# Kernel optimization log

Hardware: AMD Instinct MI355X
Metric: run time of the kernel (lower is better)

Reference implementation:

```python
import jax, jax.numpy as jnp
import numpy as np

N_NODES = 500_000
N_EDGES = 8_000_000
N_GRAPHS = 1000


def _mlp(x, w1, b1, w2, b2):
    # Linear -> SELU -> Linear (torch Sequential equivalent)
    return jax.nn.selu(x @ w1 + b1) @ w2 + b2


def setup_inputs() -> dict:
    key = jax.random.key(0)
    ks = jax.random.split(key, 25)
    p = lambda i, shape: jax.random.normal(ks[i], shape, jnp.float32) * 0.1
    return {
        "nodes": jax.random.normal(ks[0], (N_NODES, 1), jnp.float32),
        "edges": jax.random.normal(ks[1], (N_EDGES, 1), jnp.float32),
        "senders": jax.random.randint(ks[2], (N_EDGES,), 0, N_NODES),
        "receivers": jax.random.randint(ks[3], (N_EDGES,), 0, N_NODES),
        "graph_ids": jnp.sort(jax.random.randint(ks[4], (N_NODES,), 0, N_GRAPHS)),
        "num_graphs": N_GRAPHS,
        # permutate_nodes: 2 -> 10 -> 10
        "pn_w1": p(5, (2, 10)), "pn_b1": p(6, (10,)), "pn_w2": p(7, (10, 10)), "pn_b2": p(8, (10,)),
        # update_edges: 11 -> 5 -> 1
        "ue_w1": p(9, (11, 5)), "ue_b1": p(10, (5,)), "ue_w2": p(11, (5, 1)), "ue_b2": p(12, (1,)),
        # permutate_edges: 1 -> 5 -> 10
        "pe_w1": p(13, (1, 5)), "pe_b1": p(14, (5,)), "pe_w2": p(15, (5, 10)), "pe_b2": p(16, (10,)),
        # update_nodes: 11 -> 5 -> 1
        "un_w1": p(17, (11, 5)), "un_b1": p(18, (5,)), "un_w2": p(19, (5, 1)), "un_b2": p(20, (1,)),
        # predict: 11 -> 10 -> 10
        "pr_w1": p(21, (11, 10)), "pr_b1": p(22, (10,)), "pr_w2": p(23, (10, 10)), "pr_b2": p(24, (10,)),
    }


def reference(nodes, edges, pn_w1, pn_b1, pn_w2, pn_b2,
              ue_w1, ue_b1, ue_w2, ue_b2,
              pe_w1, pe_b1, pe_w2, pe_b2,
              un_w1, un_b1, un_w2, un_b2,
              pr_w1, pr_b1, pr_w2, pr_b2,
              senders, receivers, graph_ids, num_graphs):
    # gather node feats to edges: [recv || send] -> (E, 2)
    collected = jnp.concatenate([nodes[receivers], nodes[senders]], axis=-1)
    h1_nodes = _mlp(collected, pn_w1, pn_b1, pn_w2, pn_b2)  # (E, 10)
    h1_edges = edges  # (E, 1)
    for _ in range(3):
        h1_edges = _mlp(jnp.concatenate([h1_edges, h1_nodes], axis=-1),
                        ue_w1, ue_b1, ue_w2, ue_b2)  # (E, 1)
    # edges -> nodes aggregation (sum over receiver)
    edges_of_nodes = jax.ops.segment_sum(h1_edges, receivers, num_segments=nodes.shape[0])  # (N, 1)
    h2_edges = _mlp(edges_of_nodes, pe_w1, pe_b1, pe_w2, pe_b2)  # (N, 10)
    h2_nodes = nodes  # (N, 1)
    for _ in range(3):
        h2_nodes = _mlp(jnp.concatenate([h2_nodes, h2_edges], axis=-1),
                        un_w1, un_b1, un_w2, un_b2)  # (N, 1)
    # nodes -> globals aggregation (sum per graph)
    g = jax.ops.segment_sum(jnp.concatenate([h2_nodes, h2_edges], axis=-1),
                            graph_ids, num_segments=num_graphs)  # (G, 11)
    out = _mlp(g, pr_w1, pr_b1, pr_w2, pr_b2)  # (G, 10)
    return jax.nn.softmax(out, axis=-1)
```

## Files before the change

kernel.cpp:

```cpp
#include <hip/hip_runtime.h>
#include <hip/hip_fp16.h>
#include <math.h>

#define N_NODES_C  500000
#define N_EDGES_C  8000000
#define N_GRAPHS_C 1000
#define NGROUPS_C  (N_EDGES_C / 4)

#define BSHIFT  11
#define BWIDTH  2048
#define NBKT    245
#define PART_TPB 512
#define EPB     16384
#define GPB     (EPB / 4)
#define NPB     ((NGROUPS_C + GPB - 1) / GPB)
#define SROW    496
#define RITER   (GPB / PART_TPB)

#define G_BSHIFT 10
#define G_BWIDTH 1024
#define G_NBKT   489
#define NBROW    490
#define P2_TPB  512
#define EPB2    8192
#define GPB2    (EPB2 / 4)
#define NPB2    ((NGROUPS_C + GPB2 - 1) / GPB2)
#define SROW2   992
#define RITER2  (GPB2 / P2_TPB)

#define GRAPH_ACC_OFF 0
#define PARTIALS_OFF  11008
#define FW_OFF        33024
#define ZERO_HEAD     33024

#define STARTS_OFF    33280
#define PAIRS_OFF     (STARTS_OFF + 246 * SROW)
#define WS_WORDS_NEEDED (PAIRS_OFF + NPB * EPB)

#define STARTS2_OFF   33280
#define STARTS2_WORDS ((NBROW * SROW2) / 2)
#define PAIRS64_OFF   (STARTS2_OFF + STARTS2_WORDS)
#define WS2_WORDS_NEEDED (PAIRS64_OFF + NPB2 * EPB2 * 2)

#define OLD_NODE_ACC_OFF 33536
#define OLD_ZERO_WORDS   (OLD_NODE_ACC_OFF + N_NODES_C)

#define LOG2E_F 1.4426950408889634f


__device__ __forceinline__ float selu2(float xl) {
    const float C1 = 0.7282901039f;
    const float C2 = 1.7580993408473766f;
    float e = __builtin_amdgcn_exp2f(xl);
    float neg = fmaf(C2, e, -C2);
    return xl > 0.0f ? C1 * xl : neg;
}

__device__ __forceinline__ float selu_f(float x) {
    const float scale = 1.0507009873554805f;
    const float sa    = 1.0507009873554805f * 1.6732632423543772f;
    float neg = sa * (__expf(x) - 1.0f);
    return x > 0.0f ? scale * x : neg;
}

__device__ __forceinline__ void atomAddF(float* p, float v) {
    __hip_atomic_fetch_add(p, v, __ATOMIC_RELAXED, __HIP_MEMORY_SCOPE_AGENT);
}

__device__ __forceinline__ void fuse_weights(
        int t,
        const float* __restrict__ pn_w1, const float* __restrict__ pn_b1,
        const float* __restrict__ pn_w2, const float* __restrict__ pn_b2,
        const float* __restrict__ ue_w1, const float* __restrict__ ue_b1,
        const float* __restrict__ ue_w2, const float* __restrict__ ue_b2,
        const float* __restrict__ pe_w1, const float* __restrict__ pe_b1,
        const float* __restrict__ pe_w2, const float* __restrict__ pe_b2,
        const float* __restrict__ un_w1, const float* __restrict__ un_b1,
        const float* __restrict__ un_w2, const float* __restrict__ un_b2,
        float* __restrict__ fw) {
    const float L = LOG2E_F;
    if (t < 20) fw[0 + t] = pn_w1[t] * L;
    if (t < 10) fw[20 + t] = pn_b1[t] * L;
    if (t < 50) {
        int j = t / 5, k = t % 5;
        float s = 0.0f;
        for (int m = 0; m < 10; ++m) s += pn_w2[j * 10 + m] * ue_w1[(1 + m) * 5 + k];
        fw[30 + t] = s * L;
    }
    if (t < 5) {
        float s = ue_b1[t];
        for (int m = 0; m < 10; ++m) s += pn_b2[m] * ue_w1[(1 + m) * 5 + t];
        fw[80 + t] = s * L;
    }
    if (t < 5)  fw[85 + t]  = ue_w1[t] * L;
    if (t < 5)  fw[90 + t]  = ue_w2[t];
    if (t == 0) fw[95]      = ue_b2[0];
    if (t < 5)  fw[96 + t]  = pe_w1[t] * L;
    if (t < 5)  fw[101 + t] = pe_b1[t] * L;
    if (t < 50) fw[106 + t] = pe_w2[t];
    if (t < 10) fw[156 + t] = pe_b2[t];
    if (t < 25) {
        int j = t / 5, k = t % 5;
        float s = 0.0f;
        for (int m = 0; m < 10; ++m) s += pe_w2[j * 10 + m] * un_w1[(1 + m) * 5 + k];
        fw[166 + t] = s * L;
    }
    if (t < 5) {
        float s = un_b1[t];
        for (int m = 0; m < 10; ++m) s += pe_b2[m] * un_w1[(1 + m) * 5 + t];
        fw[191 + t] = s * L;
    }
    if (t < 5)  fw[196 + t] = un_w1[t] * L;
    if (t < 5)  fw[201 + t] = un_w2[t];
    if (t == 0) fw[206]     = un_b2[0];
}

__global__ __launch_bounds__(256) void k_init(
        float* __restrict__ ws,
        const float* pn_w1, const float* pn_b1, const float* pn_w2, const float* pn_b2,
        const float* ue_w1, const float* ue_b1, const float* ue_w2, const float* ue_b2,
        const float* pe_w1, const float* pe_b1, const float* pe_w2, const float* pe_b2,
        const float* un_w1, const float* un_b1, const float* un_w2, const float* un_b2) {
    int i = blockIdx.x * 256 + threadIdx.x;
    if (i < ZERO_HEAD) ws[i] = 0.0f;
    if (blockIdx.x == 0)
        fuse_weights(threadIdx.x, pn_w1, pn_b1, pn_w2, pn_b2, ue_w1, ue_b1, ue_w2, ue_b2,
                     pe_w1, pe_b1, pe_w2, pe_b2, un_w1, un_b1, un_w2, un_b2, ws + FW_OFF);
}

__global__ void k_fuse(const float* pn_w1, const float* pn_b1, const float* pn_w2, const float* pn_b2,
                       const float* ue_w1, const float* ue_b1, const float* ue_w2, const float* ue_b2,
                       const float* pe_w1, const float* pe_b1, const float* pe_w2, const float* pe_b2,
                       const float* un_w1, const float* un_b1, const float* un_w2, const float* un_b2,
                       float* fw) {
    fuse_weights(threadIdx.x, pn_w1, pn_b1, pn_w2, pn_b2, ue_w1, ue_b1, ue_w2, ue_b2,
                 pe_w1, pe_b1, pe_w2, pe_b2, un_w1, un_b1, un_w2, un_b2, fw);
}

__global__ void k_final(const float* __restrict__ graph_acc,
                        const float* __restrict__ partials,
                        const float* __restrict__ pr_w1, const float* __restrict__ pr_b1,
                        const float* __restrict__ pr_w2, const float* __restrict__ pr_b2,
                        float* __restrict__ out) {
    int g = blockIdx.x * blockDim.x + threadIdx.x;
    if (g >= N_GRAPHS_C) return;
    float gv[11];
#pragma unroll
    for (int f = 0; f < 11; ++f)
        gv[f] = graph_acc[g * 11 + f] + partials[g * 11 + f] + partials[11000 + g * 11 + f];
    float h[10];
#pragma unroll
    for (int j = 0; j < 10; ++j) {
        float z = pr_b1[j];
#pragma unroll
        for (int f = 0; f < 11; ++f) z = fmaf(gv[f], pr_w1[f * 10 + j], z);
        h[j] = selu_f(z);
    }
    float o[10];
    float mx = -1e30f;
#pragma unroll
    for (int j = 0; j < 10; ++j) {
        float z = pr_b2[j];
#pragma unroll
        for (int m = 0; m < 10; ++m) z = fmaf(h[m], pr_w2[m * 10 + j], z);
        o[j] = z;
        mx = fmaxf(mx, z);
    }
    float sum = 0.0f;
#pragma unroll
    for (int j = 0; j < 10; ++j) { o[j] = __expf(o[j] - mx); sum += o[j]; }
    float inv = 1.0f / sum;
#pragma unroll
    for (int j = 0; j < 10; ++j) out[g * 10 + j] = o[j] * inv;
}


__global__ __launch_bounds__(P2_TPB) void k_part2(
        const float* __restrict__ edges,
        const int* __restrict__ senders, const int* __restrict__ receivers,
        unsigned short* __restrict__ starts16,
        unsigned long long* __restrict__ pairs64) {
    __shared__ int hist[512];
    __shared__ int cursorS[512];
    __shared__ alignas(16) unsigned long long staged[EPB2];

    int tid = threadIdx.x;
    int p   = blockIdx.x;
    int gstart = p * GPB2;
    int gnum   = NGROUPS_C - gstart;
    if (gnum > GPB2) gnum = GPB2;

    hist[tid] = 0;
    __syncthreads();

    int4 rv4[RITER2];
#pragma unroll
    for (int r = 0; r < RITER2; ++r) {
        int idx = r * P2_TPB + tid;
        int gi  = gstart + (idx < gnum ? idx : 0);
        rv4[r] = ((const int4*)receivers)[gi];
        if (idx < gnum) {
            atomicAdd(&hist[rv4[r].x >> G_BSHIFT], 1);
            atomicAdd(&hist[rv4[r].y >> G_BSHIFT], 1);
            atomicAdd(&hist[rv4[r].z >> G_BSHIFT], 1);
            atomicAdd(&hist[rv4[r].w >> G_BSHIFT], 1);
        }
    }
    __syncthreads();

    int orig = hist[tid];
    int val  = orig;
    for (int d = 1; d < 512; d <<= 1) {
        int add = (tid >= d) ? hist[tid - d] : 0;
        __syncthreads();
        if (tid >= d) { val += add; hist[tid] = val; }
        __syncthreads();
    }
    int excl = val - orig;
    cursorS[tid] = excl;
    if (tid < NBROW) starts16[(size_t)tid * SROW2 + p] = (unsigned short)excl;
    __syncthreads();

#pragma unroll
    for (int r = 0; r < RITER2; ++r) {
        int idx = r * P2_TPB + tid;
        int gi  = gstart + (idx < gnum ? idx : 0);
        float4 e4 = ((const float4*)edges)[gi];
        int4   s4 = ((const int4*)senders)[gi];
        int4   rv = rv4[r];
        if (idx < gnum) {
            int   rvv[4] = {rv.x, rv.y, rv.z, rv.w};
            int   svv[4] = {s4.x, s4.y, s4.z, s4.w};
            float evv[4] = {e4.x, e4.y, e4.z, e4.w};
#pragma unroll
            for (int u = 0; u < 4; ++u) {
                int bkt  = rvv[u] >> G_BSHIFT;
                int slot = atomicAdd(&cursorS[bkt], 1);
                unsigned long long pk =
                    ((unsigned long long)(rvv[u] & (G_BWIDTH - 1)) << 51)
                  | ((unsigned long long)(unsigned)svv[u] << 32)
                  | (unsigned long long)__float_as_uint(evv[u]);
                staged[slot] = pk;
            }
        }
    }
    __syncthreads();

    const uint4* st4 = (const uint4*)staged;
    uint4* dst = (uint4*)(pairs64 + (size_t)p * EPB2);
    int n4 = gnum * 2;
    for (int i = tid; i < n4; i += P2_TPB) dst[i] = st4[i];
}

__global__ __launch_bounds__(1024, 8) void k_gather2(
        const float* __restrict__ nodes, const int* __restrict__ graph_ids,
        const float* __restrict__ fw, const unsigned short* __restrict__ starts16,
        const unsigned long long* __restrict__ pairs64,
        float* __restrict__ graph_acc, float* __restrict__ partials) {
    __shared__ float accf[G_BWIDTH];
    __shared__ float nf[G_BWIDTH];
    __shared__ int   s0[NPB2];
    __shared__ int   pst[NPB2 + 1];
    __shared__ int   sc[1024];
    __shared__ float garr[32 * 11];
    int tid = threadIdx.x;
    int b   = blockIdx.x;

    int nodeBase = b << G_BSHIFT;
    int lastIdx  = nodeBase + G_BWIDTH;
    if (lastIdx > N_NODES_C) lastIdx = N_NODES_C;
    int lim = lastIdx - nodeBase;

    accf[tid] = 0.0f;
    nf[tid]   = (tid < lim) ? nodes[nodeBase + tid] : 0.0f;
    if (tid < 352) garr[tid] = 0.0f;

    int cntv = 0;
    if (tid < NPB2) {
        int a = (int)starts16[(size_t)b * SROW2 + tid];
        int c = (int)starts16[(size_t)(b + 1) * SROW2 + tid];
        s0[tid] = a;
        cntv = c - a;
    }
    sc[tid] = cntv;
    __syncthreads();

    int v = cntv;
    for (int d = 1; d < 1024; d <<= 1) {
        int add = (tid >= d) ? sc[tid - d] : 0;
        __syncthreads();
        if (tid >= d) { v += add; sc[tid] = v; }
        __syncthreads();
    }
    if (tid == 0) pst[0] = 0;
    if (tid < NPB2) pst[tid + 1] = v;
    __syncthreads();

    int M = pst[NPB2];

    {
        float w_pn1[20], b_pn1[10], W_eb[50], b_eb[5], w1r0[5], w2e[5];
#pragma unroll
        for (int j = 0; j < 20; ++j) w_pn1[j] = fw[j];
#pragma unroll
        for (int j = 0; j < 10; ++j) b_pn1[j] = fw[20 + j];
#pragma unroll
        for (int j = 0; j < 50; ++j) W_eb[j] = fw[30 + j];
#pragma unroll
        for (int j = 0; j < 5; ++j) b_eb[j] = fw[80 + j];
#pragma unroll
        for (int j = 0; j < 5; ++j) w1r0[j] = fw[85 + j];
#pragma unroll
        for (int j = 0; j < 5; ++j) w2e[j] = fw[90 + j];
        float b2e = fw[95];

        int i = tid;
#pragma unroll 1
        for (; i + 1024 < M; i += 2048) {
            int iA = i, iB = i + 1024;
            int loA = 0, hiA = NPB2, loB = 0, hiB = NPB2;
#pragma unroll
            for (int s = 0; s < 10; ++s) {
                int mA = (loA + hiA) >> 1;
                int mB = (loB + hiB) >> 1;
                int pA = pst[mA];
                int pB = pst[mB];
                if (pA <= iA) loA = mA; else hiA = mA;
                if (pB <= iB) loB = mB; else hiB = mB;
            }
            unsigned long long pkA =
                pairs64[(size_t)loA * EPB2 + s0[loA] + (iA - pst[loA])];
            unsigned long long pkB =
                pairs64[(size_t)loB * EPB2 + s0[loB] + (iB - pst[loB])];
            float nsA = nodes[(int)((pkA >> 32) & 0x7FFFFULL)];
            float nsB = nodes[(int)((pkB >> 32) & 0x7FFFFULL)];
            int   rlA = (int)(pkA >> 51);
            int   rlB = (int)(pkB >> 51);
            float nrA = nf[rlA];
            float nrB = nf[rlB];
            float eA  = __uint_as_float((unsigned)pkA);
            float eB  = __uint_as_float((unsigned)pkB);

            float bsA[5], bsB[5];
#pragma unroll
            for (int k = 0; k < 5; ++k) { bsA[k] = b_eb[k]; bsB[k] = b_eb[k]; }
#pragma unroll
            for (int j = 0; j < 10; ++j) {
                float zlA = fmaf(nrA, w_pn1[j], fmaf(nsA, w_pn1[10 + j], b_pn1[j]));
                float zlB = fmaf(nrB, w_pn1[j], fmaf(nsB, w_pn1[10 + j], b_pn1[j]));
                float szA = selu2(zlA);
                float szB = selu2(zlB);
#pragma unroll
                for (int k = 0; k < 5; ++k) {
                    bsA[k] = fmaf(szA, W_eb[j * 5 + k], bsA[k]);
                    bsB[k] = fmaf(szB, W_eb[j * 5 + k], bsB[k]);
                }
            }
#pragma unroll
            for (int it = 0; it < 3; ++it) {
                float aA = b2e, aB = b2e;
#pragma unroll
                for (int k = 0; k < 5; ++k) {
                    float tA = selu2(fmaf(eA, w1r0[k], bsA[k]));
                    float tB = selu2(fmaf(eB, w1r0[k], bsB[k]));
                    aA = fmaf(tA, w2e[k], aA);
                    aB = fmaf(tB, w2e[k], aB);
                }
                eA = aA; eB = aB;
            }
            atomicAdd(&accf[rlA], eA);
            atomicAdd(&accf[rlB], eB);
        }
#pragma unroll 1
        for (; i < M; i += 1024) {
            int lo = 0, hi = NPB2;
#pragma unroll
            for (int s = 0; s < 10; ++s) {
                int mid = (lo + hi) >> 1;
                if (pst[mid] <= i) lo = mid; else hi = mid;
            }
            unsigned long long pk =
                pairs64[(size_t)lo * EPB2 + s0[lo] + (i - pst[lo])];
            int   rl   = (int)(pk >> 51);
            int   sidx = (int)((pk >> 32) & 0x7FFFFULL);
            float e    = __uint_as_float((unsigned)pk);
            float nr   = nf[rl];
            float ns   = nodes[sidx];

            float bs[5];
#pragma unroll
            for (int k = 0; k < 5; ++k) bs[k] = b_eb[k];
#pragma unroll
            for (int j = 0; j < 10; ++j) {
                float zl = fmaf(nr, w_pn1[j], fmaf(ns, w_pn1[10 + j], b_pn1[j]));
                float sz = selu2(zl);
#pragma unroll
                for (int k = 0; k < 5; ++k) bs[k] = fmaf(sz, W_eb[j * 5 + k], bs[k]);
            }
#pragma unroll
            for (int it = 0; it < 3; ++it) {
                float acc2 = b2e;
#pragma unroll
                for (int k = 0; k < 5; ++k) {
                    float tt = selu2(fmaf(e, w1r0[k], bs[k]));
                    acc2 = fmaf(tt, w2e[k], acc2);
                }
                e = acc2;
            }
            atomicAdd(&accf[rl], e);
        }
    }
    __syncthreads();

    float w_pe1[5], b_pe1[5], pe_w2[50], pe_b2[10], W_nb[25], b_nb[5], w1r0n[5], w2n[5];
#pragma unroll
    for (int j = 0; j < 5; ++j) w_pe1[j] = fw[96 + j];
#pragma unroll
    for (int j = 0; j < 5; ++j) b_pe1[j] = fw[101 + j];
#pragma unroll
    for (int j = 0; j < 50; ++j) pe_w2[j] = fw[106 + j];
#pragma unroll
    for (int j = 0; j < 10; ++j) pe_b2[j] = fw[156 + j];
#pragma unroll
    for (int j = 0; j < 25; ++j) W_nb[j] = fw[166 + j];
#pragma unroll
    for (int j = 0; j < 5; ++j) b_nb[j] = fw[191 + j];
#pragma unroll
    for (int j = 0; j < 5; ++j) w1r0n[j] = fw[196 + j];
#pragma unroll
    for (int j = 0; j < 5; ++j) w2n[j] = fw[201 + j];
    float b2n = fw[206];

    int gidBase = graph_ids[nodeBase];
    int gidEnd  = graph_ids[lastIdx - 1];

    {
        int i = nodeBase + tid;
        bool valid = tid < lim;

        float s = accf[tid];
        float t5[5];
#pragma unroll
        for (int k = 0; k < 5; ++k) t5[k] = selu2(fmaf(s, w_pe1[k], b_pe1[k]));
        float he[10];
#pragma unroll
        for (int m = 0; m < 10; ++m) {
            float a = pe_b2[m];
#pragma unroll
            for (int k = 0; k < 5; ++k) a = fmaf(t5[k], pe_w2[k * 10 + m], a);
            he[m] = a;
        }
        float bs[5];
#pragma unroll
        for (int k = 0; k < 5; ++k) {
            float a = b_nb[k];
#pragma unroll
            for (int t = 0; t < 5; ++t) a = fmaf(t5[t], W_nb[t * 5 + k], a);
            bs[k] = a;
        }
        float n = valid ? nf[tid] : 0.0f;
#pragma unroll
        for (int it = 0; it < 3; ++it) {
            float a = b2n;
#pragma unroll
            for (int k = 0; k < 5; ++k) {
                float tt = selu2(fmaf(n, w1r0n[k], bs[k]));
                a = fmaf(tt, w2n[k], a);
            }
            n = a;
        }

        int gid = valid ? graph_ids[i] : -1;
        if (!valid) {
            n = 0.0f;
#pragma unroll
            for (int m = 0; m < 10; ++m) he[m] = 0.0f;
        }

        int gid0 = __shfl(gid, 0, 64);
        bool allsame = __all(gid == gid0) && (gid0 >= 0);
        if (allsame) {
            float vv = n;
#pragma unroll
            for (int off = 32; off > 0; off >>= 1) vv += __shfl_down(vv, off, 64);
            float vh[10];
#pragma unroll
            for (int m = 0; m < 10; ++m) {
                float ww = he[m];
#pragma unroll
                for (int off = 32; off > 0; off >>= 1) ww += __shfl_down(ww, off, 64);
                vh[m] = ww;
            }
            if ((tid & 63) == 0) {
                int off = gid0 - gidBase;
                if (off >= 0 && off < 32) {
                    atomicAdd(&garr[off * 11 + 0], vv);
#pragma unroll
                    for (int m = 0; m < 10; ++m) atomicAdd(&garr[off * 11 + 1 + m], vh[m]);
                } else {
                    atomAddF(&graph_acc[gid0 * 11 + 0], vv);
#pragma unroll
                    for (int m = 0; m < 10; ++m) atomAddF(&graph_acc[gid0 * 11 + 1 + m], vh[m]);
                }
            }
        } else if (valid) {
            int off = gid - gidBase;
            if (off >= 0 && off < 32) {
                atomicAdd(&garr[off * 11 + 0], n);
#pragma unroll
                for (int m = 0; m < 10; ++m) atomicAdd(&garr[off * 11 + 1 + m], he[m]);
            } else {
                atomAddF(&graph_acc[gid * 11 + 0], n);
#pragma unroll
                for (int m = 0; m < 10; ++m) atomAddF(&graph_acc[gid * 11 + 1 + m], he[m]);
            }
        }
    }
    __syncthreads();

    int ngl = gidEnd - gidBase + 1;
    if (ngl > 32) ngl = 32;
    int par = (b & 1) * 11000;
    for (int t = tid; t < ngl * 11; t += 1024) {
        int off = t / 11, f = t - off * 11;
        partials[par + (gidBase + off) * 11 + f] = garr[t];
    }
}


__global__ __launch_bounds__(PART_TPB, 4) void k_part(
        const float* __restrict__ nodes, const float* __restrict__ edges,
        const int* __restrict__ senders, const int* __restrict__ receivers,
        const float* __restrict__ fw, int* __restrict__ starts_T,
        unsigned int* __restrict__ pairs) {
    __shared__ int hist[256];
    __shared__ int cursorS[256];
    __shared__ unsigned int staged[EPB];

    int tid = threadIdx.x;
    int p   = blockIdx.x;
    int gstart = p * GPB;
    int gnum   = NGROUPS_C - gstart;
    if (gnum > GPB) gnum = GPB;

    float w_pn1[20], b_pn1[10], W_eb[50], b_eb[5], w1r0[5], w2e[5];
#pragma unroll
    for (int j = 0; j < 20; ++j) w_pn1[j] = fw[j];
#pragma unroll
    for (int j = 0; j < 10; ++j) b_pn1[j] = fw[20 + j];
#pragma unroll
    for (int j = 0; j < 50; ++j) W_eb[j] = fw[30 + j];
#pragma unroll
    for (int j = 0; j < 5; ++j) b_eb[j] = fw[80 + j];
#pragma unroll
    for (int j = 0; j < 5; ++j) w1r0[j] = fw[85 + j];
#pragma unroll
    for (int j = 0; j < 5; ++j) w2e[j] = fw[90 + j];
    float b2e = fw[95];

    if (tid < 256) hist[tid] = 0;
    __syncthreads();

#pragma unroll 1
    for (int r = 0; r < RITER; ++r) {
        int idx = r * PART_TPB + tid;
        int gi  = gstart + (idx < gnum ? idx : 0);
        int4 rv = ((const int4*)receivers)[gi];
        if (idx < gnum) {
            atomicAdd(&hist[rv.x >> BSHIFT], 1);
            atomicAdd(&hist[rv.y >> BSHIFT], 1);
            atomicAdd(&hist[rv.z >> BSHIFT], 1);
            atomicAdd(&hist[rv.w >> BSHIFT], 1);
        }
    }
    __syncthreads();

    int orig = 0, val = 0;
    if (tid < 256) { orig = hist[tid]; val = orig; }
    for (int d = 1; d < 256; d <<= 1) {
        int add = 0;
        if (tid >= d && tid < 256) add = hist[tid - d];
        __syncthreads();
        if (tid >= d && tid < 256) { val += add; hist[tid] = val; }
        __syncthreads();
    }
    int excl = val - orig;
    if (tid < 256) cursorS[tid] = excl;
    if (tid < 246) starts_T[tid * SROW + p] = excl;
    __syncthreads();

    float4 e4A, e4B, e4N;
    int4   s4A, s4B, s4N, r4A, r4B, r4N;
    float  nsA0, nsA1, nsA2, nsA3, nrA0, nrA1, nrA2, nrA3;
    float  nsB0, nsB1, nsB2, nsB3, nrB0, nrB1, nrB2, nrB3;

    {
        int gi0 = gstart + (tid < gnum ? tid : 0);
        e4A = ((const float4*)edges)[gi0];
        s4A = ((const int4*)senders)[gi0];
        r4A = ((const int4*)receivers)[gi0];
        nsA0 = nodes[s4A.x]; nsA1 = nodes[s4A.y];
        nsA2 = nodes[s4A.z]; nsA3 = nodes[s4A.w];
        nrA0 = nodes[r4A.x]; nrA1 = nodes[r4A.y];
        nrA2 = nodes[r4A.z]; nrA3 = nodes[r4A.w];
        int idx1 = PART_TPB + tid;
        int gi1 = gstart + (idx1 < gnum ? idx1 : 0);
        e4B = ((const float4*)edges)[gi1];
        s4B = ((const int4*)senders)[gi1];
        r4B = ((const int4*)receivers)[gi1];
    }

#pragma unroll 1
    for (int r = 0; r < RITER; ++r) {
        {
            int idx2 = (r + 2) * PART_TPB + tid;
            int gi2  = gstart + (idx2 < gnum ? idx2 : 0);
            e4N = ((const float4*)edges)[gi2];
            s4N = ((const int4*)senders)[gi2];
            r4N = ((const int4*)receivers)[gi2];
        }
        nsB0 = nodes[s4B.x]; nsB1 = nodes[s4B.y];
        nsB2 = nodes[s4B.z]; nsB3 = nodes[s4B.w];
        nrB0 = nodes[r4B.x]; nrB1 = nodes[r4B.y];
        nrB2 = nodes[r4B.z]; nrB3 = nodes[r4B.w];

        float ev[4]  = {e4A.x, e4A.y, e4A.z, e4A.w};
        int   rv[4]  = {r4A.x, r4A.y, r4A.z, r4A.w};
        float nsv[4] = {nsA0, nsA1, nsA2, nsA3};
        float nrv[4] = {nrA0, nrA1, nrA2, nrA3};

        bool validr = (r * PART_TPB + tid) < gnum;
#pragma unroll
        for (int u = 0; u < 4; ++u) {
            float nr = nrv[u], ns = nsv[u];
            float bs[5];
#pragma unroll
            for (int k = 0; k < 5; ++k) bs[k] = b_eb[k];
#pragma unroll
            for (int j = 0; j < 10; ++j) {
                float zl = fmaf(nr, w_pn1[j], fmaf(ns, w_pn1[10 + j], b_pn1[j]));
                float sz = selu2(zl);
#pragma unroll
                for (int k = 0; k < 5; ++k) bs[k] = fmaf(sz, W_eb[j * 5 + k], bs[k]);
            }
            float e = ev[u];
#pragma unroll
            for (int it = 0; it < 3; ++it) {
                float acc2 = b2e;
#pragma unroll
                for (int k = 0; k < 5; ++k) {
                    float tt = selu2(fmaf(e, w1r0[k], bs[k]));
                    acc2 = fmaf(tt, w2e[k], acc2);
                }
                e = acc2;
            }
            if (validr) {
                int bkt  = rv[u] >> BSHIFT;
                int slot = atomicAdd(&cursorS[bkt], 1);
                unsigned int pk = ((unsigned int)(rv[u] & (BWIDTH - 1)) << 16)
                                | (unsigned int)__half_as_ushort(__float2half_rn(e));
                staged[slot] = pk;
            }
        }

        e4A = e4B; s4A = s4B; r4A = r4B;
        nsA0 = nsB0; nsA1 = nsB1; nsA2 = nsB2; nsA3 = nsB3;
        nrA0 = nrB0; nrA1 = nrB1; nrA2 = nrB2; nrA3 = nrB3;
        e4B = e4N; s4B = s4N; r4B = r4N;
    }
    __syncthreads();

    const uint4* staged4 = (const uint4*)staged;
    uint4* dst = (uint4*)(pairs + (size_t)p * EPB);
    for (int i = tid; i < gnum; i += PART_TPB) dst[i] = staged4[i];
}

__global__ __launch_bounds__(1024) void k_gather(
        const float* __restrict__ nodes, const int* __restrict__ graph_ids,
        const float* __restrict__ fw, const int* __restrict__ starts_T,
        const unsigned int* __restrict__ pairs, float* __restrict__ graph_acc,
        float* __restrict__ partials) {
    __shared__ float accf[BWIDTH];
    __shared__ int s0[SROW], s1[SROW];
    __shared__ float garr[32 * 11];
    int tid = threadIdx.x;
    int b   = blockIdx.x;

    accf[tid] = 0.0f; accf[1024 + tid] = 0.0f;
    if (tid < 352) garr[tid] = 0.0f;
    for (int i = tid; i < NPB; i += 1024) {
        s0[i] = starts_T[b * SROW + i];
        s1[i] = starts_T[(b + 1) * SROW + i];
    }
    __syncthreads();

    int g32 = tid >> 5, lane = tid & 31;
    for (int p = g32; p < NPB; p += 32) {
        int st = s0[p], en = s1[p];
        const unsigned int* seg = pairs + (size_t)p * EPB + st;
        int cnt = en - st;
        for (int i = lane; i < cnt; i += 32) {
            unsigned int pk = seg[i];
            atomicAdd(&accf[(pk >> 16) & (BWIDTH - 1)],
                      __half2float(__ushort_as_half((unsigned short)(pk & 0xffff))));
        }
    }
    __syncthreads();

    float w_pe1[5], b_pe1[5], pe_w2[50], pe_b2[10], W_nb[25], b_nb[5], w1r0n[5], w2n[5];
#pragma unroll
    for (int j = 0; j < 5; ++j) w_pe1[j] = fw[96 + j];
#pragma unroll
    for (int j = 0; j < 5; ++j) b_pe1[j] = fw[101 + j];
#pragma unroll
    for (int j = 0; j < 50; ++j) pe_w2[j] = fw[106 + j];
#pragma unroll
    for (int j = 0; j < 10; ++j) pe_b2[j] = fw[156 + j];
#pragma unroll
    for (int j = 0; j < 25; ++j) W_nb[j] = fw[166 + j];
#pragma unroll
    for (int j = 0; j < 5; ++j) b_nb[j] = fw[191 + j];
#pragma unroll
    for (int j = 0; j < 5; ++j) w1r0n[j] = fw[196 + j];
#pragma unroll
    for (int j = 0; j < 5; ++j) w2n[j] = fw[201 + j];
    float b2n = fw[206];

    int nodeBase = b << BSHIFT;
    int lastIdx  = nodeBase + BWIDTH;
    if (lastIdx > N_NODES_C) lastIdx = N_NODES_C;
    int gidBase = graph_ids[nodeBase];
    int gidEnd  = graph_ids[lastIdx - 1];

#pragma unroll
    for (int q = 0; q < 2; ++q) {
        int local = q * 1024 + tid;
        int i = nodeBase + local;
        bool valid = i < N_NODES_C;

        float s = accf[local];
        float t5[5];
#pragma unroll
        for (int k = 0; k < 5; ++k) t5[k] = selu2(fmaf(s, w_pe1[k], b_pe1[k]));
        float he[10];
#pragma unroll
        for (int m = 0; m < 10; ++m) {
            float a = pe_b2[m];
#pragma unroll
            for (int k = 0; k < 5; ++k) a = fmaf(t5[k], pe_w2[k * 10 + m], a);
            he[m] = a;
        }
        float bs[5];
#pragma unroll
        for (int k = 0; k < 5; ++k) {
            float a = b_nb[k];
#pragma unroll
            for (int t = 0; t < 5; ++t) a = fmaf(t5[t], W_nb[t * 5 + k], a);
            bs[k] = a;
        }
        float n = valid ? nodes[i] : 0.0f;
#pragma unroll
        for (int it = 0; it < 3; ++it) {
            float a = b2n;
#pragma unroll
            for (int k = 0; k < 5; ++k) {
                float tt = selu2(fmaf(n, w1r0n[k], bs[k]));
                a = fmaf(tt, w2n[k], a);
            }
            n = a;
        }

        int gid = valid ? graph_ids[i] : -1;
        if (!valid) {
            n = 0.0f;
#pragma unroll
            for (int m = 0; m < 10; ++m) he[m] = 0.0f;
        }

        int gid0 = __shfl(gid, 0, 64);
        bool allsame = __all(gid == gid0) && (gid0 >= 0);
        if (allsame) {
            float v = n;
#pragma unroll
            for (int off = 32; off > 0; off >>= 1) v += __shfl_down(v, off, 64);
            float vh[10];
#pragma unroll
            for (int m = 0; m < 10; ++m) {
                float ww = he[m];
#pragma unroll
                for (int off = 32; off > 0; off >>= 1) ww += __shfl_down(ww, off, 64);
                vh[m] = ww;
            }
            if ((tid & 63) == 0) {
                int off = gid0 - gidBase;
                if (off >= 0 && off < 32) {
                    atomicAdd(&garr[off * 11 + 0], v);
#pragma unroll
                    for (int m = 0; m < 10; ++m) atomicAdd(&garr[off * 11 + 1 + m], vh[m]);
                } else {
                    atomAddF(&graph_acc[gid0 * 11 + 0], v);
#pragma unroll
                    for (int m = 0; m < 10; ++m) atomAddF(&graph_acc[gid0 * 11 + 1 + m], vh[m]);
                }
            }
        } else if (valid) {
            int off = gid - gidBase;
            if (off >= 0 && off < 32) {
                atomicAdd(&garr[off * 11 + 0], n);
#pragma unroll
                for (int m = 0; m < 10; ++m) atomicAdd(&garr[off * 11 + 1 + m], he[m]);
            } else {
                atomAddF(&graph_acc[gid * 11 + 0], n);
#pragma unroll
                for (int m = 0; m < 10; ++m) atomAddF(&graph_acc[gid * 11 + 1 + m], he[m]);
            }
        }
    }
    __syncthreads();

    int ngl = gidEnd - gidBase + 1;
    if (ngl > 32) ngl = 32;
    int par = (b & 1) * 11000;
    for (int t = tid; t < ngl * 11; t += 1024) {
        int off = t / 11, f = t - off * 11;
        partials[par + (gidBase + off) * 11 + f] = garr[t];
    }
}


__global__ __launch_bounds__(256) void k_zero(float* __restrict__ ws, int len4) {
    int i = blockIdx.x * 256 + threadIdx.x;
    if (i < len4) ((float4*)ws)[i] = make_float4(0.f, 0.f, 0.f, 0.f);
}

__global__ __launch_bounds__(256) void k_edges(
        const float* __restrict__ nodes, const float* __restrict__ edges,
        const int* __restrict__ senders, const int* __restrict__ receivers,
        const float* __restrict__ fw, float* __restrict__ node_acc) {
    float w_pn1[20], b_pn1[10], W_eb[50], b_eb[5], w1r0[5], w2e[5];
#pragma unroll
    for (int j = 0; j < 20; ++j) w_pn1[j] = fw[j];
#pragma unroll
    for (int j = 0; j < 10; ++j) b_pn1[j] = fw[20 + j];
#pragma unroll
    for (int j = 0; j < 50; ++j) W_eb[j] = fw[30 + j];
#pragma unroll
    for (int j = 0; j < 5; ++j) b_eb[j] = fw[80 + j];
#pragma unroll
    for (int j = 0; j < 5; ++j) w1r0[j] = fw[85 + j];
#pragma unroll
    for (int j = 0; j < 5; ++j) w2e[j] = fw[90 + j];
    float b2e = fw[95];

    int g = blockIdx.x * 256 + threadIdx.x;
    if (g >= NGROUPS_C) return;

    float4 e4 = ((const float4*)edges)[g];
    int4  s4 = ((const int4*)senders)[g];
    int4  r4 = ((const int4*)receivers)[g];
    float ev[4] = {e4.x, e4.y, e4.z, e4.w};
    int   sv[4] = {s4.x, s4.y, s4.z, s4.w};
    int   rv[4] = {r4.x, r4.y, r4.z, r4.w};
    float nsv[4], nrv[4];
#pragma unroll
    for (int u = 0; u < 4; ++u) { nsv[u] = nodes[sv[u]]; nrv[u] = nodes[rv[u]]; }
#pragma unroll
    for (int u = 0; u < 4; ++u) {
        float nr = nrv[u], ns = nsv[u];
        float bs[5];
#pragma unroll
        for (int k = 0; k < 5; ++k) bs[k] = b_eb[k];
#pragma unroll
        for (int j = 0; j < 10; ++j) {
            float zl = fmaf(nr, w_pn1[j], fmaf(ns, w_pn1[10 + j], b_pn1[j]));
            float sz = selu2(zl);
#pragma unroll
            for (int k = 0; k < 5; ++k) bs[k] = fmaf(sz, W_eb[j * 5 + k], bs[k]);
        }
        float e = ev[u];
#pragma unroll
        for (int it = 0; it < 3; ++it) {
            float acc2 = b2e;
#pragma unroll
            for (int k = 0; k < 5; ++k) {
                float tt = selu2(fmaf(e, w1r0[k], bs[k]));
                acc2 = fmaf(tt, w2e[k], acc2);
            }
            e = acc2;
        }
        atomAddF(&node_acc[rv[u]], e);
    }
}

__global__ __launch_bounds__(256) void k_nodes(
        const float* __restrict__ nodes, const int* __restrict__ graph_ids,
        const float* __restrict__ fw, const float* __restrict__ node_acc,
        float* __restrict__ graph_acc) {
    float w_pe1[5], b_pe1[5], pe_w2[50], pe_b2[10], W_nb[25], b_nb[5], w1r0n[5], w2n[5];
#pragma unroll
    for (int j = 0; j < 5; ++j) w_pe1[j] = fw[96 + j];
#pragma unroll
    for (int j = 0; j < 5; ++j) b_pe1[j] = fw[101 + j];
#pragma unroll
    for (int j = 0; j < 50; ++j) pe_w2[j] = fw[106 + j];
#pragma unroll
    for (int j = 0; j < 10; ++j) pe_b2[j] = fw[156 + j];
#pragma unroll
    for (int j = 0; j < 25; ++j) W_nb[j] = fw[166 + j];
#pragma unroll
    for (int j = 0; j < 5; ++j) b_nb[j] = fw[191 + j];
#pragma unroll
    for (int j = 0; j < 5; ++j) w1r0n[j] = fw[196 + j];
#pragma unroll
    for (int j = 0; j < 5; ++j) w2n[j] = fw[201 + j];
    float b2n = fw[206];

    int i = blockIdx.x * 256 + threadIdx.x;
    bool valid = i < N_NODES_C;
    int ii = valid ? i : (N_NODES_C - 1);

    float s = node_acc[ii];
    float t5[5];
#pragma unroll
    for (int k = 0; k < 5; ++k) t5[k] = selu2(fmaf(s, w_pe1[k], b_pe1[k]));
    float he[10];
#pragma unroll
    for (int m = 0; m < 10; ++m) {
        float a = pe_b2[m];
#pragma unroll
        for (int k = 0; k < 5; ++k) a = fmaf(t5[k], pe_w2[k * 10 + m], a);
        he[m] = a;
    }
    float bs[5];
#pragma unroll
    for (int k = 0; k < 5; ++k) {
        float a = b_nb[k];
#pragma unroll
        for (int t = 0; t < 5; ++t) a = fmaf(t5[t], W_nb[t * 5 + k], a);
        bs[k] = a;
    }
    float n = nodes[ii];
#pragma unroll
    for (int it = 0; it < 3; ++it) {
        float a = b2n;
#pragma unroll
        for (int k = 0; k < 5; ++k) {
            float tt = selu2(fmaf(n, w1r0n[k], bs[k]));
            a = fmaf(tt, w2n[k], a);
        }
        n = a;
    }

    int gid = valid ? graph_ids[ii] : -1;
    if (!valid) {
        n = 0.0f;
#pragma unroll
        for (int m = 0; m < 10; ++m) he[m] = 0.0f;
    }

    int gid0 = __shfl(gid, 0, 64);
    bool allsame = __all(gid == gid0) && (gid0 >= 0);
    if (allsame) {
        float v = n;
#pragma unroll
        for (int off = 32; off > 0; off >>= 1) v += __shfl_down(v, off, 64);
        float vh[10];
#pragma unroll
        for (int m = 0; m < 10; ++m) {
            float ww = he[m];
#pragma unroll
            for (int off = 32; off > 0; off >>= 1) ww += __shfl_down(ww, off, 64);
            vh[m] = ww;
        }
        if ((threadIdx.x & 63) == 0) {
            atomAddF(&graph_acc[gid0 * 11 + 0], v);
#pragma unroll
            for (int m = 0; m < 10; ++m) atomAddF(&graph_acc[gid0 * 11 + 1 + m], vh[m]);
        }
    } else if (valid) {
        atomAddF(&graph_acc[gid * 11 + 0], n);
#pragma unroll
        for (int m = 0; m < 10; ++m) atomAddF(&graph_acc[gid * 11 + 1 + m], he[m]);
    }
}


extern "C" void kernel_launch(void* const* d_in, const int* in_sizes, int n_in,
                              void* d_out, int out_size, void* d_ws, size_t ws_size,
                              hipStream_t stream) {
    const float* nodes     = (const float*)d_in[0];
    const float* edges     = (const float*)d_in[1];
    const int*   senders   = (const int*)d_in[2];
    const int*   receivers = (const int*)d_in[3];
    const int*   graph_ids = (const int*)d_in[4];
    const float* pn_w1 = (const float*)d_in[6];
    const float* pn_b1 = (const float*)d_in[7];
    const float* pn_w2 = (const float*)d_in[8];
    const float* pn_b2 = (const float*)d_in[9];
    const float* ue_w1 = (const float*)d_in[10];
    const float* ue_b1 = (const float*)d_in[11];
    const float* ue_w2 = (const float*)d_in[12];
    const float* ue_b2 = (const float*)d_in[13];
    const float* pe_w1 = (const float*)d_in[14];
    const float* pe_b1 = (const float*)d_in[15];
    const float* pe_w2 = (const float*)d_in[16];
    const float* pe_b2 = (const float*)d_in[17];
    const float* un_w1 = (const float*)d_in[18];
    const float* un_b1 = (const float*)d_in[19];
    const float* un_w2 = (const float*)d_in[20];
    const float* un_b2 = (const float*)d_in[21];
    const float* pr_w1 = (const float*)d_in[22];
    const float* pr_b1 = (const float*)d_in[23];
    const float* pr_w2 = (const float*)d_in[24];
    const float* pr_b2 = (const float*)d_in[25];

    float* ws        = (float*)d_ws;
    float* graph_acc = ws + GRAPH_ACC_OFF;
    float* partials  = ws + PARTIALS_OFF;
    float* fw        = ws + FW_OFF;
    float* outp      = (float*)d_out;

    if (ws_size >= (size_t)WS2_WORDS_NEEDED * 4) {
        unsigned short* starts16 = (unsigned short*)((int*)ws + STARTS2_OFF);
        unsigned long long* pairs64 = (unsigned long long*)((int*)ws + PAIRS64_OFF);

        hipLaunchKernelGGL(k_init, dim3((ZERO_HEAD + 255) / 256), dim3(256), 0, stream, ws,
                           pn_w1, pn_b1, pn_w2, pn_b2, ue_w1, ue_b1, ue_w2, ue_b2,
                           pe_w1, pe_b1, pe_w2, pe_b2, un_w1, un_b1, un_w2, un_b2);
        hipLaunchKernelGGL(k_part2, dim3(NPB2), dim3(P2_TPB), 0, stream,
                           edges, senders, receivers, starts16, pairs64);
        hipLaunchKernelGGL(k_gather2, dim3(G_NBKT), dim3(1024), 0, stream,
                           nodes, graph_ids, fw, starts16, pairs64, graph_acc, partials);
        hipLaunchKernelGGL(k_final, dim3((N_GRAPHS_C + 255) / 256), dim3(256), 0, stream,
                           graph_acc, partials, pr_w1, pr_b1, pr_w2, pr_b2, outp);
    } else if (ws_size >= (size_t)WS_WORDS_NEEDED * 4) {
        int* starts_T        = (int*)ws + STARTS_OFF;
        unsigned int* pairs  = (unsigned int*)ws + PAIRS_OFF;

        hipLaunchKernelGGL(k_init, dim3((ZERO_HEAD + 255) / 256), dim3(256), 0, stream, ws,
                           pn_w1, pn_b1, pn_w2, pn_b2, ue_w1, ue_b1, ue_w2, ue_b2,
                           pe_w1, pe_b1, pe_w2, pe_b2, un_w1, un_b1, un_w2, un_b2);
        hipLaunchKernelGGL(k_part, dim3(NPB), dim3(PART_TPB), 0, stream,
                           nodes, edges, senders, receivers, fw, starts_T, pairs);
        hipLaunchKernelGGL(k_gather, dim3(NBKT), dim3(1024), 0, stream,
                           nodes, graph_ids, fw, starts_T, pairs, graph_acc, partials);
        hipLaunchKernelGGL(k_final, dim3((N_GRAPHS_C + 255) / 256), dim3(256), 0, stream,
                           graph_acc, partials, pr_w1, pr_b1, pr_w2, pr_b2, outp);
    } else {
        float* node_acc = ws + OLD_NODE_ACC_OFF;
        int len4 = OLD_ZERO_WORDS / 4;
        hipLaunchKernelGGL(k_zero, dim3((len4 + 255) / 256), dim3(256), 0, stream, ws, len4);
        hipLaunchKernelGGL(k_fuse, dim3(1), dim3(64), 0, stream,
                           pn_w1, pn_b1, pn_w2, pn_b2, ue_w1, ue_b1, ue_w2, ue_b2,
                           pe_w1, pe_b1, pe_w2, pe_b2, un_w1, un_b1, un_w2, un_b2, fw);
        hipLaunchKernelGGL(k_edges, dim3((NGROUPS_C + 255) / 256), dim3(256), 0, stream,
                           nodes, edges, senders, receivers, fw, node_acc);
        hipLaunchKernelGGL(k_nodes, dim3((N_NODES_C + 255) / 256), dim3(256), 0, stream,
                           nodes, graph_ids, fw, node_acc, graph_acc);
        hipLaunchKernelGGL(k_final, dim3((N_GRAPHS_C + 255) / 256), dim3(256), 0, stream,
                           graph_acc, partials, pr_w1, pr_b1, pr_w2, pr_b2, outp);
    }
}
```

Measured before the change: 331.4 us.

## Replace per-block partitioned edge layout with global bucket-contiguous scatter

Adds a global histogram pass and a single-block scan so the partition kernel can atomically claim a contiguous slot range per bucket and scatter its staged edges directly into a globally bucket-sorted array. The gather kernel then reads each bucket's edges as one contiguous range, dropping the per-block starts table, its 1024-wide prefix scan and the per-edge binary search. The cost is an extra full read of receivers, two more kernel launches, global atomics per block and bucket, and a scattered (less coalesced) write in the partition kernel, which now does a binary search per element.

Measured after the change: 338.0 us. 1.02x slower.

```diff
diff --git a/kernel.cpp b/kernel.cpp
--- a/kernel.cpp
+++ b/kernel.cpp
@@ -20,13 +20,11 @@
 #define G_BSHIFT 10
 #define G_BWIDTH 1024
 #define G_NBKT   489
-#define NBROW    490
-#define P2_TPB  512
-#define EPB2    8192
-#define GPB2    (EPB2 / 4)
-#define NPB2    ((NGROUPS_C + GPB2 - 1) / GPB2)
-#define SROW2   992
-#define RITER2  (GPB2 / P2_TPB)
+#define P3_TPB  512
+#define EPB3    8192
+#define GPB3    (EPB3 / 4)
+#define NPB3    ((NGROUPS_C + GPB3 - 1) / GPB3)
+#define RITER3  (GPB3 / P3_TPB)
 
 #define GRAPH_ACC_OFF 0
 #define PARTIALS_OFF  11008
@@ -37,10 +35,11 @@
 #define PAIRS_OFF     (STARTS_OFF + 246 * SROW)
 #define WS_WORDS_NEEDED (PAIRS_OFF + NPB * EPB)
 
-#define STARTS2_OFF   33280
-#define STARTS2_WORDS ((NBROW * SROW2) / 2)
-#define PAIRS64_OFF   (STARTS2_OFF + STARTS2_WORDS)
-#define WS2_WORDS_NEEDED (PAIRS64_OFF + NPB2 * EPB2 * 2)
+#define GTOT_OFF   33248
+#define GCUR_OFF   33760
+#define RPFX_OFF   34272
+#define PAIRS3_OFF 34784
+#define WS3_WORDS_NEEDED (PAIRS3_OFF + N_EDGES_C * 2)
 
 #define OLD_NODE_ACC_OFF 33536
 #define OLD_ZERO_WORDS   (OLD_NODE_ACC_OFF + N_NODES_C)
@@ -123,6 +122,8 @@
         const float* un_w1, const float* un_b1, const float* un_w2, const float* un_b2) {
     int i = blockIdx.x * 256 + threadIdx.x;
     if (i < ZERO_HEAD) ws[i] = 0.0f;
+    int* gtot = (int*)ws + GTOT_OFF;
+    if (i < 512) gtot[i] = 0;
     if (blockIdx.x == 0)
         fuse_weights(threadIdx.x, pn_w1, pn_b1, pn_w2, pn_b2, ue_w1, ue_b1, ue_w2, ue_b2,
                      pe_w1, pe_b1, pe_w2, pe_b2, un_w1, un_b1, un_w2, un_b2, ws + FW_OFF);
@@ -175,28 +176,76 @@
 }
 
 
-__global__ __launch_bounds__(P2_TPB) void k_part2(
+__global__ __launch_bounds__(P3_TPB) void k_hist(
+        const int* __restrict__ receivers, int* __restrict__ gtot) {
+    __shared__ int hist[512];
+    int tid = threadIdx.x, p = blockIdx.x;
+    int gstart = p * GPB3;
+    int gnum   = NGROUPS_C - gstart;
+    if (gnum > GPB3) gnum = GPB3;
+    hist[tid] = 0;
+    __syncthreads();
+#pragma unroll
+    for (int r = 0; r < RITER3; ++r) {
+        int idx = r * P3_TPB + tid;
+        int gi  = gstart + (idx < gnum ? idx : 0);
+        int4 rv = ((const int4*)receivers)[gi];
+        if (idx < gnum) {
+            atomicAdd(&hist[rv.x >> G_BSHIFT], 1);
+            atomicAdd(&hist[rv.y >> G_BSHIFT], 1);
+            atomicAdd(&hist[rv.z >> G_BSHIFT], 1);
+            atomicAdd(&hist[rv.w >> G_BSHIFT], 1);
+        }
+    }
+    __syncthreads();
+    int h = hist[tid];
+    if (h) atomicAdd(&gtot[tid], h);
+}
+
+__global__ __launch_bounds__(512) void k_rowscan(
+        const int* __restrict__ gtot, int* __restrict__ gcursor,
+        int* __restrict__ rowprefix) {
+    __shared__ int sc[512];
+    int tid = threadIdx.x;
+    int v = (tid < G_NBKT) ? gtot[tid] : 0;
+    sc[tid] = v;
+    __syncthreads();
+    int val = v;
+    for (int d = 1; d < 512; d <<= 1) {
+        int add = (tid >= d) ? sc[tid - d] : 0;
+        __syncthreads();
+        if (tid >= d) { val += add; sc[tid] = val; }
+        __syncthreads();
+    }
+    int excl = val - v;
+    gcursor[tid]  = excl;
+    rowprefix[tid] = excl;
+    if (tid == G_NBKT - 1) rowprefix[G_NBKT] = val;
+}
+
+__global__ __launch_bounds__(P3_TPB, 4) void k_part3(
         const float* __restrict__ edges,
         const int* __restrict__ senders, const int* __restrict__ receivers,
-        unsigned short* __restrict__ starts16,
-        unsigned long long* __restrict__ pairs64) {
+        int* __restrict__ gcursor, unsigned long long* __restrict__ pairs64) {
     __shared__ int hist[512];
-    __shared__ int cursorS[512];
-    __shared__ alignas(16) unsigned long long staged[EPB2];
-
-    int tid = threadIdx.x;
-    int p   = blockIdx.x;
-    int gstart = p * GPB2;
+    __shared__ int cursor[512];
+    __shared__ int lstartS[512];
+    __shared__ int segbase[512];
+    __shared__ alignas(16) unsigned long long staged[EPB3];
+
+    int tid = threadIdx.x, p = blockIdx.x;
+    int gstart = p * GPB3;
     int gnum   = NGROUPS_C - gstart;
-    if (gnum > GPB2) gnum = GPB2;
+    if (gnum > GPB3) gnum = GPB3;
+    int E = gnum * 4;
 
     hist[tid] = 0;
     __syncthreads();
 
-    int4 rv4[RITER2];
-#pragma unroll
-    for (int r = 0; r < RITER2; ++r) {
-        int idx = r * P2_TPB + tid;
+    int4 rv4[RITER3];
+#pragma unroll
+    for (int r = 0; r < RITER3; ++r) {
+        int idx = r * P3_TPB + tid;
         int gi  = gstart + (idx < gnum ? idx : 0);
         rv4[r] = ((const int4*)receivers)[gi];
         if (idx < gnum) {
@@ -208,8 +257,7 @@
     }
     __syncthreads();
 
-    int orig = hist[tid];
-    int val  = orig;
+    int orig = hist[tid], val = orig;
     for (int d = 1; d < 512; d <<= 1) {
         int add = (tid >= d) ? hist[tid - d] : 0;
         __syncthreads();
@@ -217,13 +265,18 @@
         __syncthreads();
     }
     int excl = val - orig;
-    cursorS[tid] = excl;
-    if (tid < NBROW) starts16[(size_t)tid * SROW2 + p] = (unsigned short)excl;
-    __syncthreads();
-
-#pragma unroll
-    for (int r = 0; r < RITER2; ++r) {
-        int idx = r * P2_TPB + tid;
+    cursor[tid]  = excl;
+    lstartS[tid] = excl;
+    __syncthreads();
+
+    if (tid < G_NBKT) {
+        int cnt = ((tid + 1 < 512) ? lstartS[tid + 1] : E) - excl;
+        segbase[tid] = atomicAdd(&gcursor[tid], cnt);
+    }
+
+#pragma unroll
+    for (int r = 0; r < RITER3; ++r) {
+        int idx = r * P3_TPB + tid;
         int gi  = gstart + (idx < gnum ? idx : 0);
         float4 e4 = ((const float4*)edges)[gi];
         int4   s4 = ((const int4*)senders)[gi];
@@ -235,7 +288,7 @@
 #pragma unroll
             for (int u = 0; u < 4; ++u) {
                 int bkt  = rvv[u] >> G_BSHIFT;
-                int slot = atomicAdd(&cursorS[bkt], 1);
+                int slot = atomicAdd(&cursor[bkt], 1);
                 unsigned long long pk =
                     ((unsigned long long)(rvv[u] & (G_BWIDTH - 1)) << 51)
                   | ((unsigned long long)(unsigned)svv[u] << 32)
@@ -246,22 +299,25 @@
     }
     __syncthreads();
 
-    const uint4* st4 = (const uint4*)staged;
-    uint4* dst = (uint4*)(pairs64 + (size_t)p * EPB2);
-    int n4 = gnum * 2;
-    for (int i = tid; i < n4; i += P2_TPB) dst[i] = st4[i];
-}
-
-__global__ __launch_bounds__(1024, 8) void k_gather2(
+#pragma unroll 2
+    for (int i = tid; i < E; i += P3_TPB) {
+        int lo = 0, hi = 512;
+#pragma unroll
+        for (int s = 0; s < 9; ++s) {
+            int mid = (lo + hi) >> 1;
+            if (lstartS[mid] <= i) lo = mid; else hi = mid;
+        }
+        pairs64[(size_t)segbase[lo] + (i - lstartS[lo])] = staged[i];
+    }
+}
+
+__global__ __launch_bounds__(1024, 8) void k_gather3(
         const float* __restrict__ nodes, const int* __restrict__ graph_ids,
-        const float* __restrict__ fw, const unsigned short* __restrict__ starts16,
+        const float* __restrict__ fw, const int* __restrict__ rowprefix,
         const unsigned long long* __restrict__ pairs64,
         float* __restrict__ graph_acc, float* __restrict__ partials) {
     __shared__ float accf[G_BWIDTH];
     __shared__ float nf[G_BWIDTH];
-    __shared__ int   s0[NPB2];
-    __shared__ int   pst[NPB2 + 1];
-    __shared__ int   sc[1024];
     __shared__ float garr[32 * 11];
     int tid = threadIdx.x;
     int b   = blockIdx.x;
@@ -274,29 +330,9 @@
     accf[tid] = 0.0f;
     nf[tid]   = (tid < lim) ? nodes[nodeBase + tid] : 0.0f;
     if (tid < 352) garr[tid] = 0.0f;
-
-    int cntv = 0;
-    if (tid < NPB2) {
-        int a = (int)starts16[(size_t)b * SROW2 + tid];
-        int c = (int)starts16[(size_t)(b + 1) * SROW2 + tid];
-        s0[tid] = a;
-        cntv = c - a;
-    }
-    sc[tid] = cntv;
-    __syncthreads();
-
-    int v = cntv;
-    for (int d = 1; d < 1024; d <<= 1) {
-        int add = (tid >= d) ? sc[tid - d] : 0;
-        __syncthreads();
-        if (tid >= d) { v += add; sc[tid] = v; }
-        __syncthreads();
-    }
-    if (tid == 0) pst[0] = 0;
-    if (tid < NPB2) pst[tid + 1] = v;
-    __syncthreads();
-
-    int M = pst[NPB2];
+    int base = rowprefix[b];
+    int end  = rowprefix[b + 1];
+    __syncthreads();
 
     {
         float w_pn1[20], b_pn1[10], W_eb[50], b_eb[5], w1r0[5], w2e[5];
@@ -314,24 +350,11 @@
         for (int j = 0; j < 5; ++j) w2e[j] = fw[90 + j];
         float b2e = fw[95];
 
-        int i = tid;
+        int i = base + tid;
 #pragma unroll 1
-        for (; i + 1024 < M; i += 2048) {
-            int iA = i, iB = i + 1024;
-            int loA = 0, hiA = NPB2, loB = 0, hiB = NPB2;
-#pragma unroll
-            for (int s = 0; s < 10; ++s) {
-                int mA = (loA + hiA) >> 1;
-                int mB = (loB + hiB) >> 1;
-                int pA = pst[mA];
-                int pB = pst[mB];
-                if (pA <= iA) loA = mA; else hiA = mA;
-                if (pB <= iB) loB = mB; else hiB = mB;
-            }
-            unsigned long long pkA =
-                pairs64[(size_t)loA * EPB2 + s0[loA] + (iA - pst[loA])];
-            unsigned long long pkB =
-                pairs64[(size_t)loB * EPB2 + s0[loB] + (iB - pst[loB])];
+        for (; i + 1024 < end; i += 2048) {
+            unsigned long long pkA = pairs64[i];
+            unsigned long long pkB = pairs64[i + 1024];
             float nsA = nodes[(int)((pkA >> 32) & 0x7FFFFULL)];
             float nsB = nodes[(int)((pkB >> 32) & 0x7FFFFULL)];
             int   rlA = (int)(pkA >> 51);
@@ -372,15 +395,8 @@
             atomicAdd(&accf[rlB], eB);
         }
 #pragma unroll 1
-        for (; i < M; i += 1024) {
-            int lo = 0, hi = NPB2;
-#pragma unroll
-            for (int s = 0; s < 10; ++s) {
-                int mid = (lo + hi) >> 1;
-                if (pst[mid] <= i) lo = mid; else hi = mid;
-            }
-            unsigned long long pk =
-                pairs64[(size_t)lo * EPB2 + s0[lo] + (i - pst[lo])];
+        for (; i < end; i += 1024) {
+            unsigned long long pk = pairs64[i];
             int   rl   = (int)(pk >> 51);
             int   sidx = (int)((pk >> 32) & 0x7FFFFULL);
             float e    = __uint_as_float((unsigned)pk);
@@ -1020,17 +1036,23 @@
     float* fw        = ws + FW_OFF;
     float* outp      = (float*)d_out;
 
-    if (ws_size >= (size_t)WS2_WORDS_NEEDED * 4) {
-        unsigned short* starts16 = (unsigned short*)((int*)ws + STARTS2_OFF);
-        unsigned long long* pairs64 = (unsigned long long*)((int*)ws + PAIRS64_OFF);
+    if (ws_size >= (size_t)WS3_WORDS_NEEDED * 4) {
+        int* gtot      = (int*)ws + GTOT_OFF;
+        int* gcursor   = (int*)ws + GCUR_OFF;
+        int* rowprefix = (int*)ws + RPFX_OFF;
+        unsigned long long* pairs64 = (unsigned long long*)((int*)ws + PAIRS3_OFF);
 
         hipLaunchKernelGGL(k_init, dim3((ZERO_HEAD + 255) / 256), dim3(256), 0, stream, ws,
                            pn_w1, pn_b1, pn_w2, pn_b2, ue_w1, ue_b1, ue_w2, ue_b2,
                            pe_w1, pe_b1, pe_w2, pe_b2, un_w1, un_b1, un_w2, un_b2);
-        hipLaunchKernelGGL(k_part2, dim3(NPB2), dim3(P2_TPB), 0, stream,
-                           edges, senders, receivers, starts16, pairs64);
-        hipLaunchKernelGGL(k_gather2, dim3(G_NBKT), dim3(1024), 0, stream,
-                           nodes, graph_ids, fw, starts16, pairs64, graph_acc, partials);
+        hipLaunchKernelGGL(k_hist, dim3(NPB3), dim3(P3_TPB), 0, stream,
+                           receivers, gtot);
+        hipLaunchKernelGGL(k_rowscan, dim3(1), dim3(512), 0, stream,
+                           gtot, gcursor, rowprefix);
+        hipLaunchKernelGGL(k_part3, dim3(NPB3), dim3(P3_TPB), 0, stream,
+                           edges, senders, receivers, gcursor, pairs64);
+        hipLaunchKernelGGL(k_gather3, dim3(G_NBKT), dim3(1024), 0, stream,
+                           nodes, graph_ids, fw, rowprefix, pairs64, graph_acc, partials);
         hipLaunchKernelGGL(k_final, dim3((N_GRAPHS_C + 255) / 256), dim3(256), 0, stream,
                            graph_acc, partials, pr_w1, pr_b1, pr_w2, pr_b2, outp);
     } else if (ws_size >= (size_t)WS_WORDS_NEEDED * 4) {
```
